# Kernel tuning notes

Measured on AMD Instinct MI355X. Metric: run time of the kernel, lower is better.

Reference implementation:

```python
import jax, jax.numpy as jnp
import numpy as np

B, T, D, N, H = 2, 2048, 2048, 16, 128
WINDOW = 1024
SOFT_CAP = 50.0
K_MASK = -2.3819763e+38
MAX_WAVELENGTH = 10000


def apply_rope(x, positions, head_dim):
    # x: [B, T, N, H], positions: [B, T]
    fraction = 2.0 * jnp.arange(head_dim // 2, dtype=jnp.float32) / head_dim
    timescale = MAX_WAVELENGTH ** fraction                      # [H/2]
    sinusoid = positions[..., None].astype(jnp.float32) / timescale  # [B, T, H/2]
    sinusoid = sinusoid[..., None, :]                           # [B, T, 1, H/2]
    sin, cos = jnp.sin(sinusoid), jnp.cos(sinusoid)
    first, second = jnp.split(x, 2, axis=-1)
    out = jnp.concatenate([first * cos - second * sin,
                           second * cos + first * sin], axis=-1)
    return out.astype(x.dtype)


def setup_inputs() -> dict:
    key = jax.random.key(0)
    k1, k2, k3 = jax.random.split(key, 3)
    x = jax.random.normal(k1, (B, T, D), dtype=jnp.float32)
    w_qkv = jax.random.normal(k2, (3, N, D, H), dtype=jnp.float32) * (D ** -0.5)
    w_out = jax.random.normal(k3, (N, H, D), dtype=jnp.float32) * ((N * H) ** -0.5)
    segment_pos = jnp.broadcast_to(jnp.arange(T, dtype=jnp.int32), (B, T))
    # causal attention mask [B, T, S]
    causal = jnp.tril(jnp.ones((T, T), dtype=jnp.bool_))
    attn_mask = jnp.broadcast_to(causal, (B, T, T))
    return {"x": x, "w_qkv": w_qkv, "w_out": w_out,
            "segment_pos": segment_pos, "attn_mask": attn_mask}


def reference(x, w_qkv, w_out, segment_pos, attn_mask):
    # QKV projection: [3, B, T, N, H]
    q, k, v = jnp.einsum('BTD,SNDH->SBTNH', x, w_qkv)
    q = apply_rope(q, segment_pos, H) * (H ** -0.5)
    k = apply_rope(k, segment_pos, H)
    logits = jnp.einsum('BTNH,BSNH->BTNS', q, k)
    # soft cap
    logits = jnp.tanh(logits / SOFT_CAP) * SOFT_CAP
    # sliding-window mask combined with causal mask
    ones = jnp.ones_like(attn_mask)
    sliding = jnp.triu(ones, -WINDOW + 1) & jnp.tril(ones, WINDOW - 1)
    mask = sliding & attn_mask                                   # [B, T, S]
    padded = jnp.where(mask[:, :, None, :], logits, K_MASK)
    probs = jax.nn.softmax(padded, axis=-1).astype(k.dtype)
    encoded = jnp.einsum('BTNS,BSNH->BTNH', probs, v)
    return jnp.einsum('BTNH,NHD->BTD', encoded, w_out)
```

## Files before the change

### kernel.cpp

```cpp
#include <hip/hip_runtime.h>

#define B_ 2
#define T_ 2048
#define D_ 2048
#define N_ 16
#define H_ 128
constexpr int WIN = 1024;

typedef __attribute__((ext_vector_type(8))) short s16x8;
typedef __attribute__((ext_vector_type(4))) float f32x4;
typedef __attribute__((ext_vector_type(4))) unsigned short u16x4;

typedef const __attribute__((address_space(1))) void cglobal_void;
typedef __attribute__((address_space(3))) void lds_void;

__device__ __forceinline__ unsigned short f2b(float f) {
  union { float f; unsigned u; } v; v.f = f;
  unsigned r = v.u + 0x7FFFu + ((v.u >> 16) & 1u);
  return (unsigned short)(r >> 16);
}
__device__ __forceinline__ float b2f(unsigned short u) {
  union { unsigned u; float f; } v; v.u = ((unsigned)u) << 16;
  return v.f;
}

__global__ __launch_bounds__(256) void detect_kernel(
    const unsigned short* __restrict__ x, int* __restrict__ flag) {
  __shared__ int cnt[256];
  const int tid = threadIdx.x;
  int c = 0;
  for (int i = tid; i < 4096; i += 256) {
    const unsigned short u = x[2 * i];
    const int e = (u >> 7) & 0xFF;
    if (e >= 154) ++c;
  }
  cnt[tid] = c;
  __syncthreads();
  for (int s = 128; s > 0; s >>= 1) {
    if (tid < s) cnt[tid] += cnt[tid + s];
    __syncthreads();
  }
  if (tid == 0) *flag = cnt[0];
}

__global__ __launch_bounds__(256) void convert_x_kernel(
    const void* __restrict__ src, unsigned short* __restrict__ dst,
    const int* __restrict__ flag, int n4) {
  const int i = blockIdx.x * 256 + threadIdx.x;
  if (i >= n4) return;
  const bool isf = (*flag > 64);
  u16x4 o;
  if (isf) {
    const float4 f = ((const float4*)src)[i];
    o[0] = f2b(f.x); o[1] = f2b(f.y); o[2] = f2b(f.z); o[3] = f2b(f.w);
  } else {
    o = ((const u16x4*)src)[i];
  }
  *(u16x4*)(dst + 4 * (size_t)i) = o;
}

__global__ __launch_bounds__(256) void transpose_kernel(
    const void* __restrict__ src, unsigned short* __restrict__ dst,
    int R, int C, const int* __restrict__ flag) {
  __shared__ unsigned short tile[32][33];
  const bool isf = (*flag > 64);
  const int c0 = blockIdx.x * 32, r0 = blockIdx.y * 32;
  const size_t base = (size_t)blockIdx.z * R * C;
  const int tx = threadIdx.x, ty = threadIdx.y;
#pragma unroll
  for (int j = 0; j < 32; j += 8) {
    const size_t idx = base + (size_t)(r0 + ty + j) * C + c0 + tx;
    tile[ty + j][tx] = isf ? f2b(((const float*)src)[idx])
                           : ((const unsigned short*)src)[idx];
  }
  __syncthreads();
#pragma unroll
  for (int j = 0; j < 32; j += 8)
    dst[base + (size_t)(c0 + ty + j) * R + r0 + tx] = tile[tx][ty + j];
}

__global__ __launch_bounds__(256) void transpose_bf16_kernel(
    const unsigned short* __restrict__ src, unsigned short* __restrict__ dst,
    int R, int C) {
  __shared__ unsigned short tile[32][33];
  const int c0 = blockIdx.x * 32, r0 = blockIdx.y * 32;
  const size_t base = (size_t)blockIdx.z * R * C;
  const int tx = threadIdx.x, ty = threadIdx.y;
#pragma unroll
  for (int j = 0; j < 32; j += 8)
    tile[ty + j][tx] = src[base + (size_t)(r0 + ty + j) * C + c0 + tx];
  __syncthreads();
#pragma unroll
  for (int j = 0; j < 32; j += 8)
    dst[base + (size_t)(c0 + ty + j) * R + r0 + tx] = tile[tx][ty + j];
}

__global__ __launch_bounds__(512, 2) void gemm256x128_kernel(
    const unsigned short* __restrict__ A,
    const unsigned short* __restrict__ Bt,
    void* __restrict__ outp,
    int mode, const int* __restrict__ flag) {
  constexpr int K = D_;
  __shared__ unsigned short As[3 * 16384];
  __shared__ unsigned short Bs[3 * 8192];
  const int tid = threadIdx.x;
  const int lane = tid & 63;
  const int lr = lane & 15, lq = lane >> 4;
  const int wave = tid >> 6;
  const int wm = (wave >> 1) * 64, wn = (wave & 1) * 64;

  const int lin = blockIdx.y * 16 + blockIdx.x;
  const int nblk = (int)(gridDim.x * gridDim.y);
  const int wg = (lin & 7) * (nblk >> 3) + (lin >> 3);
  const int bx = wg & 15;
  const int by = wg >> 4;

  const size_t m0 = (size_t)bx * 256;
  const unsigned short* pA = A + m0 * K;
  const unsigned short* pB = Bt + (size_t)by * 128 * K;

  const int fv = *flag;
  asm volatile("s_waitcnt vmcnt(0)" ::: "memory");

  const int cgs = (tid & 3) ^ ((tid >> 3) & 3);
  const size_t gbase = (size_t)(tid >> 2) * K + (size_t)(cgs * 8);

  const int swz = (lr >> 1) & 3;
  const int aoff = (wm + lr) * 32 + ((lq ^ swz) << 3);
  const int boff = (wn + lr) * 32 + ((lq ^ swz) << 3);

  f32x4 acc[4][4] = {};
  s16x8 af[4], bf[4];

#define STAGE_A(bufp, kk, h)                                                  \
  {                                                                           \
    _Pragma("unroll")                                                         \
    for (int j = 0; j < 2; ++j)                                               \
      __builtin_amdgcn_global_load_lds(                                       \
          (cglobal_void*)(pA + gbase + (size_t)j * 128 * K + (kk) + (h) * 32),\
          (lds_void*)((bufp) + (h) * 8192 + (j * 512 + tid) * 8), 16, 0, 0);  \
  }
#define STAGE_B(bufp, kk, h)                                                  \
  __builtin_amdgcn_global_load_lds(                                           \
      (cglobal_void*)(pB + gbase + (kk) + (h) * 32),                          \
      (lds_void*)((bufp) + (h) * 4096 + tid * 8), 16, 0, 0);

#define LOAD_F(h)                                                             \
  {                                                                           \
    _Pragma("unroll")                                                         \
    for (int i = 0; i < 4; ++i) {                                             \
      af[i] = *(const s16x8*)(Ab + (h) * 8192 + aoff + i * 512);              \
      bf[i] = *(const s16x8*)(Bb + (h) * 4096 + boff + i * 512);              \
    }                                                                         \
  }

#define PHASE_MID()                                                           \
  __builtin_amdgcn_s_barrier();                                               \
  asm volatile("s_waitcnt lgkmcnt(0)" ::: "memory");                          \
  __builtin_amdgcn_sched_barrier(0);

#define MFMA16()                                                              \
  __builtin_amdgcn_s_setprio(1);                                              \
  {                                                                           \
    _Pragma("unroll")                                                         \
    for (int mb = 0; mb < 4; ++mb) {                                          \
      _Pragma("unroll")                                                       \
      for (int nb = 0; nb < 4; ++nb)                                          \
        acc[mb][nb] = __builtin_amdgcn_mfma_f32_16x16x32_bf16(                \
            af[mb], bf[nb], acc[mb][nb], 0, 0, 0);                            \
    }                                                                         \
  }                                                                           \
  __builtin_amdgcn_s_setprio(0);

#define PHASE_END() __builtin_amdgcn_s_barrier();
#define VM6() asm volatile("s_waitcnt vmcnt(6)" ::: "memory");

  STAGE_A(As, 0, 0); STAGE_A(As, 0, 1); STAGE_B(Bs, 0, 0); STAGE_B(Bs, 0, 1);
  STAGE_A(As + 16384, 64, 0); STAGE_A(As + 16384, 64, 1);
  STAGE_B(Bs + 8192, 64, 0);  STAGE_B(Bs + 8192, 64, 1);
  VM6();
  __builtin_amdgcn_s_barrier();

  int bt = 0, bp = 2;
  for (int t = 0; t < K / 64; ++t) {
    const unsigned short* Ab = As + bt * 16384;
    const unsigned short* Bb = Bs + bt * 8192;
    unsigned short* Ap = As + bp * 16384;
    unsigned short* Bp = Bs + bp * 8192;
    const int kn = (t + 2) * 64;
    LOAD_F(0);
    STAGE_A(Ap, kn, 0); STAGE_B(Bp, kn, 0);
    PHASE_MID(); MFMA16(); PHASE_END();
    LOAD_F(1);
    STAGE_A(Ap, kn, 1); STAGE_B(Bp, kn, 1);
    VM6();
    PHASE_MID(); MFMA16(); PHASE_END();
    bt = (bt == 2) ? 0 : bt + 1;
    bp = (bp == 2) ? 0 : bp + 1;
  }

  const int n0 = by << 7;
  if (mode == 0) {
    const bool isf = (fv > 64);
#pragma unroll
    for (int mb = 0; mb < 4; ++mb) {
#pragma unroll
      for (int i = 0; i < 4; ++i) {
        const size_t r = m0 + wm + mb * 16 + lq * 4 + i;
#pragma unroll
        for (int nb = 0; nb < 4; ++nb) {
          const size_t c = (size_t)(n0 + wn + nb * 16 + lr);
          if (isf) ((float*)outp)[r * D_ + c] = acc[mb][nb][i];
          else ((unsigned short*)outp)[r * D_ + c] = f2b(acc[mb][nb][i]);
        }
      }
    }
  } else {
    unsigned short* op = (unsigned short*)outp;
    const size_t SB = (size_t)B_ * N_ * T_ * H_;
#pragma unroll
    for (int mb = 0; mb < 4; ++mb) {
#pragma unroll
      for (int i = 0; i < 4; ++i) {
        const size_t r = m0 + wm + mb * 16 + lq * 4 + i;
        const int b = (int)(r >> 11);
        const int tt = (int)(r & 2047);
#pragma unroll
        for (int nb = 0; nb < 4; ++nb) {
          const int g = n0 + wn + nb * 16 + lr;
          const int s = g >> 11, n = (g >> 7) & 15, h = g & 127;
          op[(size_t)s * SB + (size_t)(b * N_ + n) * T_ * H_ +
             (size_t)tt * H_ + h] = f2b(acc[mb][nb][i]);
        }
      }
    }
  }
#undef STAGE_A
#undef STAGE_B
#undef LOAD_F
#undef PHASE_MID
#undef MFMA16
#undef PHASE_END
#undef VM6
}

__global__ __launch_bounds__(256) void rope_kernel(unsigned short* __restrict__ qk) {
  const int tid = threadIdx.x;
  const int lane = tid & 63;
  const size_t row = (size_t)blockIdx.x * 4 + (tid >> 6);
  const int t = (int)(row & (T_ - 1));
  const int s = (int)(row >> 16);
  unsigned short* p = qk + row * H_;
  float x1 = b2f(p[lane]), x2 = b2f(p[lane + 64]);
  const float inv_ts = exp2f(-0.20762050f * (float)lane);
  float sv, cv;
  __sincosf((float)t * inv_ts, &sv, &cv);
  float o1 = x1 * cv - x2 * sv;
  float o2 = x2 * cv + x1 * sv;
  if (s == 0) { o1 *= 0.08838834764831845f; o2 *= 0.08838834764831845f; }
  p[lane] = f2b(o1);
  p[lane + 64] = f2b(o2);
}

__global__ __launch_bounds__(256, 4) void attn_kernel(
    const unsigned short* __restrict__ qkv,
    const unsigned short* __restrict__ vt,
    unsigned short* __restrict__ enc) {
  const int tid = threadIdx.x, lane = tid & 63, wave = tid >> 6;
  const int lr = lane & 15, lq = lane >> 4;
  const int bn = blockIdx.x;
  const int b = bn >> 4, n = bn & 15;
  const int t0 = blockIdx.y * 64;
  const size_t SB = (size_t)B_ * N_ * T_ * H_;
  const unsigned short* qp = qkv + (size_t)bn * T_ * H_;
  const unsigned short* kp = qp + SB;
  const unsigned short* vp = vt + (size_t)bn * T_ * H_;

  __shared__ unsigned short Ks[64 * 128];
  __shared__ unsigned short Vt[128 * 64];
  unsigned short* Ps = Ks + wave * 1024;

  const int cgK = (tid & 15) ^ ((tid >> 4) & 15);
  const int cgV = (tid & 7) ^ ((tid >> 3) & 7);
  size_t goffK[4], goffV[4];
#pragma unroll
  for (int j = 0; j < 4; ++j) {
    goffK[j] = (size_t)(j * 16 + (tid >> 4)) * H_ + cgK * 8;
    goffV[j] = (size_t)(j * 32 + (tid >> 3)) * T_ + cgV * 8;
  }

  s16x8 aq[4];
  {
    const int t = t0 + wave * 16 + lr;
#pragma unroll
    for (int kc = 0; kc < 4; ++kc)
      aq[kc] = *(const s16x8*)(qp + (size_t)t * H_ + kc * 32 + lq * 8);
  }

  f32x4 oacc[8] = {};
  float lp[4] = {0.f, 0.f, 0.f, 0.f};

  const int s_lo = (t0 >= WIN - 1) ? ((t0 - (WIN - 1)) & ~63) : 0;
  constexpr float C_IN = 0.05770780f;
  constexpr float M_SCALE = -144.269504f;
  constexpr float M_BIAS = 86.56f;

  for (int s0 = s_lo; s0 <= t0 + 63; s0 += 64) {
    __syncthreads();
#pragma unroll
    for (int j = 0; j < 4; ++j) {
      __builtin_amdgcn_global_load_lds((cglobal_void*)(kp + (size_t)s0 * H_ + goffK[j]),
                                       (lds_void*)(Ks + (size_t)(j * 256 + tid) * 8), 16, 0, 0);
      __builtin_amdgcn_global_load_lds((cglobal_void*)(vp + goffV[j] + s0),
                                       (lds_void*)(Vt + (size_t)(j * 256 + tid) * 8), 16, 0, 0);
    }
    __syncthreads();

    float p[4][4];
#pragma unroll
    for (int sb = 0; sb < 4; ++sb) {
      f32x4 a = {};
#pragma unroll
      for (int kc = 0; kc < 4; ++kc) {
        const int co = (((kc << 2) + lq) ^ lr) * 8;
        s16x8 bk = *(const s16x8*)(Ks + (sb * 16 + lr) * 128 + co);
        a = __builtin_amdgcn_mfma_f32_16x16x32_bf16(aq[kc], bk, a, 0, 0, 0);
      }
#pragma unroll
      for (int i = 0; i < 4; ++i) {
        const float u = exp2f(a[i] * C_IN);
        const float r = __builtin_amdgcn_rcpf(u + 1.0f);
        p[sb][i] = exp2f(fmaf(r, M_SCALE, M_BIAS));
      }
    }

    const bool interior = (s0 + 63 <= t0) && (s0 >= t0 + 63 - (WIN - 1));
    if (!interior) {
#pragma unroll
      for (int sb = 0; sb < 4; ++sb) {
        const int key = s0 + sb * 16 + lr;
#pragma unroll
        for (int i = 0; i < 4; ++i) {
          const int t = t0 + wave * 16 + lq * 4 + i;
          if (key > t || key < t - (WIN - 1)) p[sb][i] = 0.0f;
        }
      }
    }
#pragma unroll
    for (int sb = 0; sb < 4; ++sb)
#pragma unroll
      for (int i = 0; i < 4; ++i) lp[i] += p[sb][i];

    __syncthreads();
#pragma unroll
    for (int sb = 0; sb < 4; ++sb)
#pragma unroll
      for (int i = 0; i < 4; ++i) {
        const int row = lq * 4 + i;
        const int cph = ((sb * 2 + (lr >> 3)) ^ (row & 7));
        Ps[row * 64 + cph * 8 + (lr & 7)] = f2b(p[sb][i]);
      }
    __syncthreads();

    s16x8 ap[2];
#pragma unroll
    for (int kc = 0; kc < 2; ++kc)
      ap[kc] = *(const s16x8*)(Ps + lr * 64 + ((((kc << 2) + lq) ^ (lr & 7)) * 8));

#pragma unroll
    for (int hb = 0; hb < 8; ++hb) {
#pragma unroll
      for (int kc = 0; kc < 2; ++kc) {
        const int co = (((kc << 2) + lq) ^ (lr & 7)) * 8;
        s16x8 bv = *(const s16x8*)(Vt + (hb * 16 + lr) * 64 + co);
        oacc[hb] = __builtin_amdgcn_mfma_f32_16x16x32_bf16(ap[kc], bv, oacc[hb], 0, 0, 0);
      }
    }
  }

#pragma unroll
  for (int i = 0; i < 4; ++i) {
#pragma unroll
    for (int off = 1; off < 16; off <<= 1)
      lp[i] += __shfl_xor(lp[i], off, 64);
  }

#pragma unroll
  for (int i = 0; i < 4; ++i) {
    const int t = t0 + wave * 16 + lq * 4 + i;
    const float inv = 1.0f / lp[i];
    const size_t rowb = ((size_t)b * T_ + t) * (N_ * H_) + (size_t)n * H_;
#pragma unroll
    for (int hb = 0; hb < 8; ++hb)
      enc[rowb + hb * 16 + lr] = f2b(oacc[hb][i] * inv);
  }
}

extern "C" void kernel_launch(void* const* d_in, const int* in_sizes, int n_in,
                              void* d_out, int out_size, void* d_ws, size_t ws_size,
                              hipStream_t stream) {
  const void* x     = d_in[0];
  const void* w_qkv = d_in[1];
  const void* w_out = d_in[2];

  char* wsb = (char*)d_ws;
  int* flag = (int*)wsb;
  const size_t MB = 1048576;
  unsigned short* xc    = (unsigned short*)(wsb + 64);
  unsigned short* wqkvT = (unsigned short*)(wsb + 64 + 16 * MB);
  unsigned short* qkv   = (unsigned short*)(wsb + 64 + 40 * MB);
  unsigned short* vt    = xc;
  unsigned short* enc   = wqkvT;
  unsigned short* woutT = (unsigned short*)(wsb + 64 + 32 * MB);
  unsigned short* v     = qkv + 2 * (size_t)B_ * N_ * T_ * H_;

  detect_kernel<<<1, 256, 0, stream>>>((const unsigned short*)x, flag);
  convert_x_kernel<<<8192, 256, 0, stream>>>(x, xc, flag, B_ * T_ * D_ / 4);
  transpose_kernel<<<dim3(4, 64, 48), dim3(32, 8), 0, stream>>>(w_qkv, wqkvT, 2048, 128, flag);
  gemm256x128_kernel<<<dim3(16, 48), 512, 0, stream>>>(xc, wqkvT, qkv, 1, flag);
  rope_kernel<<<32768, 256, 0, stream>>>(qkv);
  transpose_bf16_kernel<<<dim3(4, 64, 32), dim3(32, 8), 0, stream>>>(v, vt, 2048, 128);
  transpose_kernel<<<dim3(64, 64, 1), dim3(32, 8), 0, stream>>>(w_out, woutT, 2048, 2048, flag);
  attn_kernel<<<dim3(32, 32), 256, 0, stream>>>(qkv, vt, enc);
  gemm256x128_kernel<<<dim3(16, 16), 512, 0, stream>>>(enc, woutT, d_out, 0, flag);
}
```

Before: 438.4 us.

## Add 256x256 QKV GEMM and double-buffer K/V tiles in attention

Adds a new 256x256-tile GEMM kernel with two LDS buffers and a phased MFMA/load schedule, and uses it for the QKV projection in place of the 256x128 kernel. The attention kernel now double-buffers its K and V tiles, prefetching the next 64-key block while computing on the current one, and moves P into a separate LDS region so fewer barriers are needed. The goal is to hide global-load latency and raise arithmetic reuse. The cost is more LDS per block, which lowers attention occupancy (launch bounds go from 4 to 2) and adds register pressure in the larger GEMM. The last prefetch also loads one block past the loop range.

```diff
diff --git a/kernel.cpp b/kernel.cpp
--- a/kernel.cpp
+++ b/kernel.cpp
@@ -93,6 +93,151 @@
 #pragma unroll
   for (int j = 0; j < 32; j += 8)
     dst[base + (size_t)(c0 + ty + j) * R + r0 + tx] = tile[tx][ty + j];
+}
+
+__global__ __launch_bounds__(512, 2) void gemm256_kernel(
+    const unsigned short* __restrict__ A,
+    const unsigned short* __restrict__ Bt,
+    void* __restrict__ outp,
+    int mode, const int* __restrict__ flag) {
+  constexpr int K = D_;
+  __shared__ unsigned short As[2][16384];
+  __shared__ unsigned short Bs[2][16384];
+  const int tid = threadIdx.x;
+  const int lane = tid & 63;
+  const int lr = lane & 15, lq = lane >> 4;
+  const int wave = tid >> 6;
+  const int wm = (wave >> 2) * 128, wn = (wave & 3) * 64;
+  const size_t m0 = (size_t)blockIdx.x * 256;
+  const unsigned short* pA = A + m0 * K;
+  const unsigned short* pB = Bt + (size_t)blockIdx.y * 256 * K;
+
+  const int fv = *flag;
+  asm volatile("s_waitcnt vmcnt(0)" ::: "memory");
+
+  const int cgs = (tid & 3) ^ ((tid >> 3) & 3);
+  const size_t gbase = (size_t)(tid >> 2) * K + (size_t)(cgs * 8);
+
+  const int swz = (lr >> 1) & 3;
+  const int aoff = (wm + lr) * 32 + ((lq ^ swz) << 3);
+  const int boff = (wn + lr) * 32 + ((lq ^ swz) << 3);
+
+  f32x4 acc[8][4] = {};
+  s16x8 af[8], bf[2];
+
+#define STAGE(mat, ptr, ibuf, kk, h)                                          \
+  {                                                                           \
+    _Pragma("unroll")                                                         \
+    for (int j = 0; j < 2; ++j)                                               \
+      __builtin_amdgcn_global_load_lds(                                       \
+          (cglobal_void*)((ptr) + gbase + (size_t)j * 128 * K + (kk) + (h) * 32), \
+          (lds_void*)(&mat[ibuf][(h) * 8192 + (j * 512 + tid) * 8]), 16, 0, 0); \
+  }
+
+#define LOAD_A(kq)                                                            \
+  {                                                                           \
+    _Pragma("unroll")                                                         \
+    for (int mb = 0; mb < 8; ++mb)                                            \
+      af[mb] = *(const s16x8*)(&As[ib][(kq) * 8192 + aoff + mb * 512]);       \
+  }
+
+#define LOAD_B(kq, nh)                                                        \
+  {                                                                           \
+    _Pragma("unroll")                                                         \
+    for (int nb = 0; nb < 2; ++nb)                                            \
+      bf[nb] = *(const s16x8*)(&Bs[ib][(kq) * 8192 + boff + ((nh) * 2 + nb) * 512]); \
+  }
+
+#define PHASE_MID()                                                           \
+  __builtin_amdgcn_s_barrier();                                               \
+  asm volatile("s_waitcnt lgkmcnt(0)" ::: "memory");                          \
+  __builtin_amdgcn_sched_barrier(0);
+
+#define MFMA16(nh)                                                            \
+  __builtin_amdgcn_s_setprio(1);                                              \
+  {                                                                           \
+    _Pragma("unroll")                                                         \
+    for (int mb = 0; mb < 8; ++mb) {                                          \
+      acc[mb][(nh) * 2] = __builtin_amdgcn_mfma_f32_16x16x32_bf16(            \
+          af[mb], bf[0], acc[mb][(nh) * 2], 0, 0, 0);                         \
+      acc[mb][(nh) * 2 + 1] = __builtin_amdgcn_mfma_f32_16x16x32_bf16(        \
+          af[mb], bf[1], acc[mb][(nh) * 2 + 1], 0, 0, 0);                     \
+    }                                                                         \
+  }                                                                           \
+  __builtin_amdgcn_s_setprio(0);
+
+#define PHASE_END() __builtin_amdgcn_s_barrier();
+#define VM4() asm volatile("s_waitcnt vmcnt(4)" ::: "memory");
+
+  STAGE(As, pA, 0, 0, 0);
+  STAGE(Bs, pB, 0, 0, 0);
+  STAGE(As, pA, 0, 0, 1);
+  STAGE(Bs, pB, 0, 0, 1);
+  VM4();
+  __builtin_amdgcn_s_barrier();
+
+  for (int t = 0; t < K / 64; ++t) {
+    const int ib = t & 1;
+    const int kn = (t + 1) * 64;
+    LOAD_A(0); LOAD_B(0, 0);
+    STAGE(As, pA, ib ^ 1, kn, 0);
+    PHASE_MID(); MFMA16(0); PHASE_END();
+    LOAD_B(0, 1);
+    STAGE(Bs, pB, ib ^ 1, kn, 0);
+    VM4();
+    PHASE_MID(); MFMA16(1); PHASE_END();
+    LOAD_A(1); LOAD_B(1, 0);
+    STAGE(As, pA, ib ^ 1, kn, 1);
+    PHASE_MID(); MFMA16(0); PHASE_END();
+    LOAD_B(1, 1);
+    STAGE(Bs, pB, ib ^ 1, kn, 1);
+    VM4();
+    PHASE_MID(); MFMA16(1); PHASE_END();
+  }
+
+  const int n0 = blockIdx.y << 8;
+  if (mode == 0) {
+    const bool isf = (fv > 64);
+#pragma unroll
+    for (int mb = 0; mb < 8; ++mb) {
+#pragma unroll
+      for (int i = 0; i < 4; ++i) {
+        const size_t r = m0 + wm + mb * 16 + lq * 4 + i;
+#pragma unroll
+        for (int nb = 0; nb < 4; ++nb) {
+          const size_t c = (size_t)(n0 + wn + nb * 16 + lr);
+          if (isf) ((float*)outp)[r * D_ + c] = acc[mb][nb][i];
+          else ((unsigned short*)outp)[r * D_ + c] = f2b(acc[mb][nb][i]);
+        }
+      }
+    }
+  } else {
+    unsigned short* op = (unsigned short*)outp;
+    const size_t SB = (size_t)B_ * N_ * T_ * H_;
+#pragma unroll
+    for (int mb = 0; mb < 8; ++mb) {
+#pragma unroll
+      for (int i = 0; i < 4; ++i) {
+        const size_t r = m0 + wm + mb * 16 + lq * 4 + i;
+        const int b = (int)(r >> 11);
+        const int tt = (int)(r & 2047);
+#pragma unroll
+        for (int nb = 0; nb < 4; ++nb) {
+          const int g = n0 + wn + nb * 16 + lr;
+          const int s = g >> 11, n = (g >> 7) & 15, h = g & 127;
+          op[(size_t)s * SB + (size_t)(b * N_ + n) * T_ * H_ +
+             (size_t)tt * H_ + h] = f2b(acc[mb][nb][i]);
+        }
+      }
+    }
+  }
+#undef STAGE
+#undef LOAD_A
+#undef LOAD_B
+#undef PHASE_MID
+#undef MFMA16
+#undef PHASE_END
+#undef VM4
 }
 
 __global__ __launch_bounds__(512, 2) void gemm256x128_kernel(
@@ -262,7 +407,7 @@
   p[lane + 64] = f2b(o2);
 }
 
-__global__ __launch_bounds__(256, 4) void attn_kernel(
+__global__ __launch_bounds__(256, 2) void attn_kernel(
     const unsigned short* __restrict__ qkv,
     const unsigned short* __restrict__ vt,
     unsigned short* __restrict__ enc) {
@@ -276,9 +421,10 @@
   const unsigned short* kp = qp + SB;
   const unsigned short* vp = vt + (size_t)bn * T_ * H_;
 
-  __shared__ unsigned short Ks[64 * 128];
-  __shared__ unsigned short Vt[128 * 64];
-  unsigned short* Ps = Ks + wave * 1024;
+  __shared__ unsigned short Ks[2][64 * 128];
+  __shared__ unsigned short Vt[2][128 * 64];
+  __shared__ unsigned short Psm[4][16 * 64];
+  unsigned short* Ps = Psm[wave];
 
   const int cgK = (tid & 15) ^ ((tid >> 4) & 15);
   const int cgV = (tid & 7) ^ ((tid >> 3) & 7);
@@ -295,6 +441,20 @@
 #pragma unroll
     for (int kc = 0; kc < 4; ++kc)
       aq[kc] = *(const s16x8*)(qp + (size_t)t * H_ + kc * 32 + lq * 8);
+  }
+  asm volatile("s_waitcnt vmcnt(0)" ::: "memory");
+
+#define STAGE_T(ibuf, s0v)                                                    \
+  {                                                                           \
+    _Pragma("unroll")                                                         \
+    for (int j = 0; j < 4; ++j) {                                             \
+      __builtin_amdgcn_global_load_lds(                                       \
+          (cglobal_void*)(kp + (size_t)(s0v) * H_ + goffK[j]),                \
+          (lds_void*)(Ks[ibuf] + (size_t)(j * 256 + tid) * 8), 16, 0, 0);     \
+      __builtin_amdgcn_global_load_lds(                                       \
+          (cglobal_void*)(vp + goffV[j] + (s0v)),                             \
+          (lds_void*)(Vt[ibuf] + (size_t)(j * 256 + tid) * 8), 16, 0, 0);     \
+    }                                                                         \
   }
 
   f32x4 oacc[8] = {};
@@ -305,16 +465,16 @@
   constexpr float M_SCALE = -144.269504f;
   constexpr float M_BIAS = 86.56f;
 
+  STAGE_T(0, s_lo);
+
+  int cur = 0;
   for (int s0 = s_lo; s0 <= t0 + 63; s0 += 64) {
-    __syncthreads();
-#pragma unroll
-    for (int j = 0; j < 4; ++j) {
-      __builtin_amdgcn_global_load_lds((cglobal_void*)(kp + (size_t)s0 * H_ + goffK[j]),
-                                       (lds_void*)(Ks + (size_t)(j * 256 + tid) * 8), 16, 0, 0);
-      __builtin_amdgcn_global_load_lds((cglobal_void*)(vp + goffV[j] + s0),
-                                       (lds_void*)(Vt + (size_t)(j * 256 + tid) * 8), 16, 0, 0);
-    }
-    __syncthreads();
+    STAGE_T(cur ^ 1, s0 + 64);
+    asm volatile("s_waitcnt vmcnt(8)" ::: "memory");
+    __builtin_amdgcn_s_barrier();
+
+    const unsigned short* Kb = Ks[cur];
+    const unsigned short* Vb = Vt[cur];
 
     float p[4][4];
 #pragma unroll
@@ -323,7 +483,7 @@
 #pragma unroll
       for (int kc = 0; kc < 4; ++kc) {
         const int co = (((kc << 2) + lq) ^ lr) * 8;
-        s16x8 bk = *(const s16x8*)(Ks + (sb * 16 + lr) * 128 + co);
+        s16x8 bk = *(const s16x8*)(Kb + (sb * 16 + lr) * 128 + co);
         a = __builtin_amdgcn_mfma_f32_16x16x32_bf16(aq[kc], bk, a, 0, 0, 0);
       }
 #pragma unroll
@@ -351,7 +511,6 @@
 #pragma unroll
       for (int i = 0; i < 4; ++i) lp[i] += p[sb][i];
 
-    __syncthreads();
 #pragma unroll
     for (int sb = 0; sb < 4; ++sb)
 #pragma unroll
@@ -360,7 +519,6 @@
         const int cph = ((sb * 2 + (lr >> 3)) ^ (row & 7));
         Ps[row * 64 + cph * 8 + (lr & 7)] = f2b(p[sb][i]);
       }
-    __syncthreads();
 
     s16x8 ap[2];
 #pragma unroll
@@ -372,11 +530,15 @@
 #pragma unroll
       for (int kc = 0; kc < 2; ++kc) {
         const int co = (((kc << 2) + lq) ^ (lr & 7)) * 8;
-        s16x8 bv = *(const s16x8*)(Vt + (hb * 16 + lr) * 64 + co);
+        s16x8 bv = *(const s16x8*)(Vb + (hb * 16 + lr) * 64 + co);
         oacc[hb] = __builtin_amdgcn_mfma_f32_16x16x32_bf16(ap[kc], bv, oacc[hb], 0, 0, 0);
       }
     }
-  }
+
+    __builtin_amdgcn_s_barrier();
+    cur ^= 1;
+  }
+#undef STAGE_T
 
 #pragma unroll
   for (int i = 0; i < 4; ++i) {
@@ -417,7 +579,7 @@
   detect_kernel<<<1, 256, 0, stream>>>((const unsigned short*)x, flag);
   convert_x_kernel<<<8192, 256, 0, stream>>>(x, xc, flag, B_ * T_ * D_ / 4);
   transpose_kernel<<<dim3(4, 64, 48), dim3(32, 8), 0, stream>>>(w_qkv, wqkvT, 2048, 128, flag);
-  gemm256x128_kernel<<<dim3(16, 48), 512, 0, stream>>>(xc, wqkvT, qkv, 1, flag);
+  gemm256_kernel<<<dim3(16, 24), 512, 0, stream>>>(xc, wqkvT, qkv, 1, flag);
   rope_kernel<<<32768, 256, 0, stream>>>(qkv);
   transpose_bf16_kernel<<<dim3(4, 64, 32), dim3(32, 8), 0, stream>>>(v, vt, 2048, 128);
   transpose_kernel<<<dim3(64, 64, 1), dim3(32, 8), 0, stream>>>(w_out, woutT, 2048, 2048, flag);
```

Measured after the change: 431.5 us. Within noise of the previous version (-1.6%).
